# Optimization experiments

Measured on AMD Instinct MI355X. Metric: run time of the kernel, lower is better.

Reference implementation:

```python
import jax, jax.numpy as jnp
import numpy as np
from jax import lax

DN = ('NCHW', 'OIHW', 'NCHW')
BN_EPS = 1e-5


def _conv(x, w, pad):
    # pad: list of (lo, hi) for H, W
    return lax.conv_general_dilated(x, w, (1, 1), pad, dimension_numbers=DN)


def _grid_sample_bilinear(img, grid):
    """F.grid_sample(img, grid, align_corners=True, padding_mode='zeros').
    img: [N,C,H,W], grid: [N,Ho,Wo,2] with (x,y) in [-1,1]."""
    N, C, H, W = img.shape
    gx, gy = grid[..., 0], grid[..., 1]
    # align_corners=True mapping to pixel coords
    ix = (gx + 1.0) * 0.5 * (W - 1)
    iy = (gy + 1.0) * 0.5 * (H - 1)
    x0 = jnp.floor(ix)
    y0 = jnp.floor(iy)
    x1 = x0 + 1.0
    y1 = y0 + 1.0
    # bilinear weights
    wa = (x1 - ix) * (y1 - iy)  # top-left (x0,y0)
    wb = (ix - x0) * (y1 - iy)  # top-right (x1,y0)
    wc = (x1 - ix) * (iy - y0)  # bottom-left (x0,y1)
    wd = (ix - x0) * (iy - y0)  # bottom-right (x1,y1)

    imgc = jnp.transpose(img, (0, 2, 3, 1))  # [N,H,W,C]
    b = jnp.arange(N)[:, None, None]

    def gather(xi, yi):
        valid = (xi >= 0) & (xi <= W - 1) & (yi >= 0) & (yi <= H - 1)
        xc = jnp.clip(xi, 0, W - 1).astype(jnp.int32)
        yc = jnp.clip(yi, 0, H - 1).astype(jnp.int32)
        v = imgc[b, yc, xc]  # [N,Ho,Wo,C]
        return v * valid[..., None].astype(img.dtype)

    out = (gather(x0, y0) * wa[..., None] + gather(x1, y0) * wb[..., None]
           + gather(x0, y1) * wc[..., None] + gather(x1, y1) * wd[..., None])
    return jnp.transpose(out, (0, 3, 1, 2))  # [N,C,Ho,Wo]


def setup_inputs() -> dict:
    key = jax.random.key(0)
    ks = jax.random.split(key, 12)
    N, C1, C2 = 8, 512, 256
    H, W = 64, 64
    x1 = jax.random.normal(ks[0], (N, C1, 2 * H, 2 * W), dtype=jnp.float32)
    x2 = jax.random.normal(ks[1], (N, C2, H, W), dtype=jnp.float32)
    w_change = jax.random.normal(ks[2], (C2, C1, 1, 1), dtype=jnp.float32) * 0.02
    b_change = jax.random.normal(ks[3], (C2,), dtype=jnp.float32) * 0.02
    w_cc1 = jax.random.normal(ks[4], (C2, 2 * C2, 1, 1), dtype=jnp.float32) * 0.02
    bn_gamma = 1.0 + 0.1 * jax.random.normal(ks[5], (C2,), dtype=jnp.float32)
    bn_beta = 0.1 * jax.random.normal(ks[6], (C2,), dtype=jnp.float32)
    bn_mean = 0.1 * jax.random.normal(ks[7], (C2,), dtype=jnp.float32)
    bn_var = jax.random.uniform(ks[8], (C2,), dtype=jnp.float32, minval=0.5, maxval=1.5)
    w_cc2 = jax.random.normal(ks[9], (4, C2, 3, 3), dtype=jnp.float32) * 0.02
    return {"x1": x1, "x2": x2, "w_change": w_change, "b_change": b_change,
            "w_cc1": w_cc1, "bn_gamma": bn_gamma, "bn_beta": bn_beta,
            "bn_mean": bn_mean, "bn_var": bn_var, "w_cc2": w_cc2}


def reference(x1, x2, w_change, b_change, w_cc1, bn_gamma, bn_beta, bn_mean, bn_var, w_cc2):
    # MaxPool2d(2,2)
    x1p = lax.reduce_window(x1, -jnp.inf, lax.max, (1, 1, 2, 2), (1, 1, 2, 2), 'VALID')
    # change: 1x1 conv with bias
    x1c = _conv(x1p, w_change, [(0, 0), (0, 0)]) + b_change[None, :, None, None]
    # concat + concat_conv (1x1 conv -> BN(eval) -> ReLU -> 3x3 conv)
    x = jnp.concatenate([x1c, x2], axis=1)
    x = _conv(x, w_cc1, [(0, 0), (0, 0)])
    inv = lax.rsqrt(bn_var + BN_EPS)
    x = (x - bn_mean[None, :, None, None]) * (inv * bn_gamma)[None, :, None, None] + bn_beta[None, :, None, None]
    x = jax.nn.relu(x)
    flow = _conv(x, w_cc2, [(1, 1), (1, 1)])  # [N,4,H,W]
    flow1 = flow[:, :2]
    flow2 = flow[:, 2:]

    N, _, H, W = x1c.shape
    # base grid: [...,0]=x over width, [...,1]=y over height
    xs = jnp.linspace(-1.0, 1.0, W, dtype=x1c.dtype)
    ys = jnp.linspace(-1.0, 1.0, H, dtype=x1c.dtype)
    base = jnp.stack(jnp.meshgrid(xs, ys, indexing='xy'), axis=-1)  # [H,W,2]
    norm = jnp.array([(W - 1) / 2.0, (H - 1) / 2.0], dtype=x1c.dtype)

    grid1 = base[None] + jnp.transpose(flow1, (0, 2, 3, 1)) / norm
    grid2 = base[None] + jnp.transpose(flow2, (0, 2, 3, 1)) / norm

    u1 = _grid_sample_bilinear(x1c, grid1)
    u2 = _grid_sample_bilinear(x2, grid2)
    return u1 + u2
```

## Files before the change

kernel.cpp:

```cpp
#include <hip/hip_runtime.h>
#include <hip/hip_bf16.h>

#define NB 8
#define C1 512
#define C2 256
#define HWSZ 4096
#define BN_EPS 1e-5f
#define P2 264

typedef __hip_bfloat16 bf16;
typedef __hip_bfloat162 bf162;
typedef __attribute__((ext_vector_type(8))) short short8v;
typedef __attribute__((ext_vector_type(4))) float f32x4;

static __device__ inline float b2f(bf16 h) { return __bfloat162float(h); }

static __device__ inline unsigned short f2bf(float f) {
  union { bf16 h; unsigned short u; } c;
  c.h = __float2bfloat16(f);
  return c.u;
}

static __device__ inline uint2 pack4(float a, float b, float c, float d) {
  union { uint2 u; bf162 h[2]; } pk;
  pk.h[0] = __float22bfloat162_rn(make_float2(a, b));
  pk.h[1] = __float22bfloat162_rn(make_float2(c, d));
  return pk.u;
}

__global__ __launch_bounds__(256) void k0_swizzle(
    const float* __restrict__ wch, const float* __restrict__ wcc1,
    unsigned short* __restrict__ wchB, unsigned short* __restrict__ wcc1B) {
  const int t = blockIdx.x * 256 + threadIdx.x;
  const int which = t >> 17;
  const int r = t & 131071;
  const int i = r & 7;
  const int lane = (r >> 3) & 63;
  const int ntile = (r >> 9) & 15;
  const int kstep = r >> 13;
  const int ci = kstep * 32 + (lane >> 4) * 8 + i;
  const int co = ntile * 16 + (lane & 15);
  const float* s = which ? wcc1 : wch;
  unsigned short* d = which ? wcc1B : wchB;
  d[r] = f2bf(s[co * 512 + ci]);
}

__global__ __launch_bounds__(256) void k12_fused(
    const float* __restrict__ x1, const float* __restrict__ x2,
    const unsigned short* __restrict__ wchB, const unsigned short* __restrict__ wcc1B,
    const float* __restrict__ bch,
    const float* __restrict__ gamma, const float* __restrict__ beta,
    const float* __restrict__ mean, const float* __restrict__ var,
    bf16* __restrict__ x1c, bf16* __restrict__ xbn) {
  __shared__ unsigned short As[32 * 40];
  __shared__ unsigned short As2[32 * P2];
  const int tid = threadIdx.x;
  const int lane = tid & 63;
  const int wv = tid >> 6;
  const int lrow = lane & 15;
  const int lgrp = lane >> 4;
  const int sm = tid & 31;
  const int skq = tid >> 5;

  const int m0g = blockIdx.x * 32;
  const int n = m0g >> 12;
  const int hw0 = m0g & 4095;
  const int h = hw0 >> 6;
  const int w0 = hw0 & 63;

  f32x4 acc[2][4];
#pragma unroll
  for (int mt = 0; mt < 2; ++mt)
#pragma unroll
    for (int nt = 0; nt < 4; ++nt) acc[mt][nt] = (f32x4){0.f, 0.f, 0.f, 0.f};

  const size_t x1base = ((size_t)n * C1 * 16384) + (size_t)(2 * h) * 128 + (size_t)(2 * (w0 + sm));

  float av[4];
#pragma unroll
  for (int j = 0; j < 4; ++j) {
    const size_t cioff = (size_t)(skq * 4 + j) * 16384;
    const float2 p0 = *(const float2*)(x1 + x1base + cioff);
    const float2 p1 = *(const float2*)(x1 + x1base + cioff + 128);
    av[j] = fmaxf(fmaxf(p0.x, p0.y), fmaxf(p1.x, p1.y));
  }

  for (int ks = 0; ks < 16; ++ks) {
    __syncthreads();
    *(uint2*)&As[sm * 40 + skq * 4] = pack4(av[0], av[1], av[2], av[3]);
    __syncthreads();

    const short8v a0 = *(const short8v*)&As[lrow * 40 + lgrp * 8];
    const short8v a1 = *(const short8v*)&As[(16 + lrow) * 40 + lgrp * 8];

    if (ks < 15) {
      const int k0 = (ks + 1) * 32;
#pragma unroll
      for (int j = 0; j < 4; ++j) {
        const size_t cioff = (size_t)(k0 + skq * 4 + j) * 16384;
        const float2 p0 = *(const float2*)(x1 + x1base + cioff);
        const float2 p1 = *(const float2*)(x1 + x1base + cioff + 128);
        av[j] = fmaxf(fmaxf(p0.x, p0.y), fmaxf(p1.x, p1.y));
      }
    }

#pragma unroll
    for (int nt = 0; nt < 4; ++nt) {
      const int ntile = wv * 4 + nt;
      const short8v b = *(const short8v*)&wchB[(size_t)((ks * 16 + ntile) * 64 + lane) * 8];
      acc[0][nt] = __builtin_amdgcn_mfma_f32_16x16x32_bf16(a0, b, acc[0][nt], 0, 0, 0);
      acc[1][nt] = __builtin_amdgcn_mfma_f32_16x16x32_bf16(a1, b, acc[1][nt], 0, 0, 0);
    }
  }

#pragma unroll
  for (int nt = 0; nt < 4; ++nt) {
    const int co = wv * 64 + nt * 16 + lrow;
    const float bias = bch[co];
#pragma unroll
    for (int mt = 0; mt < 2; ++mt) {
      const f32x4 v = acc[mt][nt];
      const uint2 pk = pack4(v.x + bias, v.y + bias, v.z + bias, v.w + bias);
      *(uint2*)&x1c[((size_t)(n * C2 + co)) * HWSZ + hw0 + mt * 16 + lgrp * 4] = pk;
      const int mb = mt * 16 + lgrp * 4;
      As2[(mb + 0) * P2 + co] = (unsigned short)(pk.x & 0xffffu);
      As2[(mb + 1) * P2 + co] = (unsigned short)(pk.x >> 16);
      As2[(mb + 2) * P2 + co] = (unsigned short)(pk.y & 0xffffu);
      As2[(mb + 3) * P2 + co] = (unsigned short)(pk.y >> 16);
      acc[mt][nt] = (f32x4){0.f, 0.f, 0.f, 0.f};
    }
  }
  __syncthreads();

  const int ch = tid >> 3;
  const int mq = (tid & 7) * 4;

  float4 cf = *(const float4*)&x2[((size_t)(n * C2 + ch)) * HWSZ + hw0 + mq];

#pragma unroll
  for (int ks = 0; ks < 8; ++ks) {
    const short8v a0 = *(const short8v*)&As2[lrow * P2 + ks * 32 + lgrp * 8];
    const short8v a1 = *(const short8v*)&As2[(16 + lrow) * P2 + ks * 32 + lgrp * 8];
#pragma unroll
    for (int nt = 0; nt < 4; ++nt) {
      const int ntile = wv * 4 + nt;
      const short8v b = *(const short8v*)&wcc1B[(size_t)((ks * 16 + ntile) * 64 + lane) * 8];
      acc[0][nt] = __builtin_amdgcn_mfma_f32_16x16x32_bf16(a0, b, acc[0][nt], 0, 0, 0);
      acc[1][nt] = __builtin_amdgcn_mfma_f32_16x16x32_bf16(a1, b, acc[1][nt], 0, 0, 0);
    }
  }

  for (int ks = 8; ks < 16; ++ks) {
    unsigned short pk[4];
    pk[0] = f2bf(cf.x); pk[1] = f2bf(cf.y); pk[2] = f2bf(cf.z); pk[3] = f2bf(cf.w);
    if (ks < 15) {
      cf = *(const float4*)&x2[((size_t)(n * C2 + (ks - 7) * 32 + ch)) * HWSZ + hw0 + mq];
    }
    __syncthreads();
    As[(mq + 0) * 40 + ch] = pk[0];
    As[(mq + 1) * 40 + ch] = pk[1];
    As[(mq + 2) * 40 + ch] = pk[2];
    As[(mq + 3) * 40 + ch] = pk[3];
    __syncthreads();

    const short8v a0 = *(const short8v*)&As[lrow * 40 + lgrp * 8];
    const short8v a1 = *(const short8v*)&As[(16 + lrow) * 40 + lgrp * 8];
#pragma unroll
    for (int nt = 0; nt < 4; ++nt) {
      const int ntile = wv * 4 + nt;
      const short8v b = *(const short8v*)&wcc1B[(size_t)((ks * 16 + ntile) * 64 + lane) * 8];
      acc[0][nt] = __builtin_amdgcn_mfma_f32_16x16x32_bf16(a0, b, acc[0][nt], 0, 0, 0);
      acc[1][nt] = __builtin_amdgcn_mfma_f32_16x16x32_bf16(a1, b, acc[1][nt], 0, 0, 0);
    }
  }

#pragma unroll
  for (int nt = 0; nt < 4; ++nt) {
    const int co = wv * 64 + nt * 16 + lrow;
    const float sc = gamma[co] * rsqrtf(var[co] + BN_EPS);
    const float sh = beta[co] - mean[co] * sc;
#pragma unroll
    for (int mt = 0; mt < 2; ++mt) {
      const f32x4 vv = acc[mt][nt];
      *(uint2*)&xbn[((size_t)(n * C2 + co)) * HWSZ + hw0 + mt * 16 + lgrp * 4] =
          pack4(fmaxf(vv.x * sc + sh, 0.f), fmaxf(vv.y * sc + sh, 0.f),
                fmaxf(vv.z * sc + sh, 0.f), fmaxf(vv.w * sc + sh, 0.f));
    }
  }
}

__global__ __launch_bounds__(1024) void k34_conv_sample(
    const bf16* __restrict__ xbn, const float* __restrict__ wcc2,
    const bf16* __restrict__ x1c, const float* __restrict__ x2,
    float* __restrict__ out) {
  __shared__ float wsm[9216];
  __shared__ float part[16][4][64];
  __shared__ float flr[4][64];
  const int tid = threadIdx.x;
  const int n = blockIdx.x >> 6;
  const int h = blockIdx.x & 63;
  const int wl = tid & 63;
  const int q = tid >> 6;

  for (int idx = tid; idx < 9216; idx += 1024) {
    const int f = idx / 2304;
    const int r = idx % 2304;
    const int ci = r / 9;
    const int t = r % 9;
    wsm[ci * 36 + (t / 3) * 12 + (t % 3) * 4 + f] = wcc2[idx];
  }
  __syncthreads();

  float acc[4] = {0.f, 0.f, 0.f, 0.f};
  {
    const bf16* base = xbn + ((size_t)(n * C2 + q * 16)) * HWSZ;
    const float* wq = wsm + (q * 16) * 36;
    for (int cc = 0; cc < 16; ++cc) {
      const bf16* src = base + (size_t)cc * HWSZ;
      const float* wc = wq + cc * 36;
#pragma unroll
      for (int dy = 0; dy < 3; ++dy) {
        const int y = h + dy - 1;
        if ((unsigned)y >= 64u) continue;
        const float v = b2f(src[y * 64 + wl]);
        float vm = __shfl_up(v, 1);
        float vp = __shfl_down(v, 1);
        if (wl == 0) vm = 0.f;
        if (wl == 63) vp = 0.f;
        const float4 wa = *(const float4*)&wc[dy * 12 + 0];
        const float4 wb = *(const float4*)&wc[dy * 12 + 4];
        const float4 wd = *(const float4*)&wc[dy * 12 + 8];
        acc[0] = fmaf(vm, wa.x, fmaf(v, wb.x, fmaf(vp, wd.x, acc[0])));
        acc[1] = fmaf(vm, wa.y, fmaf(v, wb.y, fmaf(vp, wd.y, acc[1])));
        acc[2] = fmaf(vm, wa.z, fmaf(v, wb.z, fmaf(vp, wd.z, acc[2])));
        acc[3] = fmaf(vm, wa.w, fmaf(v, wb.w, fmaf(vp, wd.w, acc[3])));
      }
    }
  }
  part[q][0][wl] = acc[0];
  part[q][1][wl] = acc[1];
  part[q][2][wl] = acc[2];
  part[q][3][wl] = acc[3];
  __syncthreads();
  if (tid < 256) {
    const int f = tid >> 6;
    const int ww = tid & 63;
    float s = 0.f;
#pragma unroll
    for (int qq = 0; qq < 16; ++qq) s += part[qq][f][ww];
    flr[f][ww] = s;
  }
  __syncthreads();

  const float fx1 = flr[0][wl];
  const float fy1 = flr[1][wl];
  const float fx2 = flr[2][wl];
  const float fy2 = flr[3][wl];

  int oA1, oB1, oC1, oD1; float wa1, wb1, wc1, wd1;
  {
    const float ix = (float)wl + fx1, iy = (float)h + fy1;
    const float x0f = floorf(ix), y0f = floorf(iy);
    const float fx = ix - x0f, fy = iy - y0f;
    const int x0 = (int)x0f, y0 = (int)y0f, x1i = x0 + 1, y1i = y0 + 1;
    const float vx0 = (x0 >= 0 && x0 < 64) ? 1.f : 0.f;
    const float vx1 = (x1i >= 0 && x1i < 64) ? 1.f : 0.f;
    const float vy0 = (y0 >= 0 && y0 < 64) ? 1.f : 0.f;
    const float vy1 = (y1i >= 0 && y1i < 64) ? 1.f : 0.f;
    const int cx0 = min(max(x0, 0), 63), cx1 = min(max(x1i, 0), 63);
    const int cy0 = min(max(y0, 0), 63), cy1 = min(max(y1i, 0), 63);
    oA1 = cy0 * 64 + cx0; oB1 = cy0 * 64 + cx1;
    oC1 = cy1 * 64 + cx0; oD1 = cy1 * 64 + cx1;
    wa1 = (1.f - fx) * (1.f - fy) * vx0 * vy0;
    wb1 = fx * (1.f - fy) * vx1 * vy0;
    wc1 = (1.f - fx) * fy * vx0 * vy1;
    wd1 = fx * fy * vx1 * vy1;
  }
  int oA2, oB2, oC2, oD2; float wa2, wb2, wc2, wd2;
  {
    const float ix = (float)wl + fx2, iy = (float)h + fy2;
    const float x0f = floorf(ix), y0f = floorf(iy);
    const float fx = ix - x0f, fy = iy - y0f;
    const int x0 = (int)x0f, y0 = (int)y0f, x1i = x0 + 1, y1i = y0 + 1;
    const float vx0 = (x0 >= 0 && x0 < 64) ? 1.f : 0.f;
    const float vx1 = (x1i >= 0 && x1i < 64) ? 1.f : 0.f;
    const float vy0 = (y0 >= 0 && y0 < 64) ? 1.f : 0.f;
    const float vy1 = (y1i >= 0 && y1i < 64) ? 1.f : 0.f;
    const int cx0 = min(max(x0, 0), 63), cx1 = min(max(x1i, 0), 63);
    const int cy0 = min(max(y0, 0), 63), cy1 = min(max(y1i, 0), 63);
    oA2 = cy0 * 64 + cx0; oB2 = cy0 * 64 + cx1;
    oC2 = cy1 * 64 + cx0; oD2 = cy1 * 64 + cx1;
    wa2 = (1.f - fx) * (1.f - fy) * vx0 * vy0;
    wb2 = fx * (1.f - fy) * vx1 * vy0;
    wc2 = (1.f - fx) * fy * vx0 * vy1;
    wd2 = fx * fy * vx1 * vy1;
  }

  const bf16*  p1 = x1c + ((size_t)n * C2) * HWSZ;
  const float* p2 = x2 + ((size_t)n * C2) * HWSZ;
  const size_t obase = ((size_t)n * C2) * HWSZ + h * 64 + wl;
#pragma unroll 4
  for (int i = 0; i < 16; ++i) {
    const int co = q * 16 + i;
    const bf16*  q1 = p1 + (size_t)co * HWSZ;
    const float* q2 = p2 + (size_t)co * HWSZ;
    const float u = b2f(q1[oA1]) * wa1 + b2f(q1[oB1]) * wb1 + b2f(q1[oC1]) * wc1 + b2f(q1[oD1]) * wd1
                  + q2[oA2] * wa2 + q2[oB2] * wb2 + q2[oC2] * wc2 + q2[oD2] * wd2;
    out[obase + (size_t)co * HWSZ] = u;
  }
}

extern "C" void kernel_launch(void* const* d_in, const int* in_sizes, int n_in,
                              void* d_out, int out_size, void* d_ws, size_t ws_size,
                              hipStream_t stream) {
  const float* x1      = (const float*)d_in[0];
  const float* x2      = (const float*)d_in[1];
  const float* w_change= (const float*)d_in[2];
  const float* b_change= (const float*)d_in[3];
  const float* w_cc1   = (const float*)d_in[4];
  const float* bn_gamma= (const float*)d_in[5];
  const float* bn_beta = (const float*)d_in[6];
  const float* bn_mean = (const float*)d_in[7];
  const float* bn_var  = (const float*)d_in[8];
  const float* w_cc2   = (const float*)d_in[9];
  float* out = (float*)d_out;

  bf16*           x1c   = (bf16*)d_ws;
  bf16*           xbn   = (bf16*)((char*)d_ws + (16u << 20));
  unsigned short* wchB  = (unsigned short*)((char*)d_ws + (32u << 20));
  unsigned short* wcc1B = (unsigned short*)((char*)d_ws + (32u << 20) + (256u << 10));

  k0_swizzle<<<1024, 256, 0, stream>>>(w_change, w_cc1, wchB, wcc1B);
  k12_fused<<<1024, 256, 0, stream>>>(x1, x2, wchB, wcc1B, b_change,
                                      bn_gamma, bn_beta, bn_mean, bn_var,
                                      x1c, xbn);
  k34_conv_sample<<<512, 1024, 0, stream>>>(xbn, w_cc2, x1c, x2, out);
}
```

Measured before the change: 150.4 us.

## Deepen x1/x2 prefetch to two stages and use raw LDS barriers in fused GEMM

```diff
diff --git a/kernel.cpp b/kernel.cpp
--- a/kernel.cpp
+++ b/kernel.cpp
@@ -21,12 +21,22 @@
   return c.u;
 }
 
+static __device__ inline unsigned pack2(float a, float b) {
+  union { unsigned u; bf162 h; } pk;
+  pk.h = __float22bfloat162_rn(make_float2(a, b));
+  return pk.u;
+}
+
 static __device__ inline uint2 pack4(float a, float b, float c, float d) {
   union { uint2 u; bf162 h[2]; } pk;
   pk.h[0] = __float22bfloat162_rn(make_float2(a, b));
   pk.h[1] = __float22bfloat162_rn(make_float2(c, d));
   return pk.u;
 }
+
+#define SBARQ() asm volatile("s_waitcnt lgkmcnt(0)\n\ts_barrier" ::: "memory")
+#define SBAR()  asm volatile("s_barrier" ::: "memory")
+#define LGKM0() asm volatile("s_waitcnt lgkmcnt(0)" ::: "memory")
 
 __global__ __launch_bounds__(256) void k0_swizzle(
     const float* __restrict__ wch, const float* __restrict__ wcc1,
@@ -59,8 +69,6 @@
   const int wv = tid >> 6;
   const int lrow = lane & 15;
   const int lgrp = lane >> 4;
-  const int sm = tid & 31;
-  const int skq = tid >> 5;
 
   const int m0g = blockIdx.x * 32;
   const int n = m0g >> 12;
@@ -74,36 +82,45 @@
 #pragma unroll
     for (int nt = 0; nt < 4; ++nt) acc[mt][nt] = (f32x4){0.f, 0.f, 0.f, 0.f};
 
-  const size_t x1base = ((size_t)n * C1 * 16384) + (size_t)(2 * h) * 128 + (size_t)(2 * (w0 + sm));
-
-  float av[4];
-#pragma unroll
-  for (int j = 0; j < 4; ++j) {
-    const size_t cioff = (size_t)(skq * 4 + j) * 16384;
-    const float2 p0 = *(const float2*)(x1 + x1base + cioff);
-    const float2 p1 = *(const float2*)(x1 + x1base + cioff + 128);
-    av[j] = fmaxf(fmaxf(p0.x, p0.y), fmaxf(p1.x, p1.y));
-  }
+  const int pmi = tid & 15;
+  const int ms = pmi * 2;
+  const int ch0 = (tid >> 4) * 2;
+
+  const float* x1p = x1 + (size_t)n * C1 * 16384 + (size_t)(2 * h) * 128 + 2 * (w0 + ms);
+
+  float4 t0, b0, t1, b1;
+#define LOADA(K0_) do { \
+    const float* p_ = x1p + (size_t)((K0_) + ch0) * 16384; \
+    t0 = *(const float4*)p_;            b0 = *(const float4*)(p_ + 128); \
+    t1 = *(const float4*)(p_ + 16384);  b1 = *(const float4*)(p_ + 16384 + 128); \
+  } while (0)
+#define POOLA(U0_, U1_) do { \
+    U0_ = pack2(fmaxf(fmaxf(t0.x, t0.y), fmaxf(b0.x, b0.y)), \
+                fmaxf(fmaxf(t1.x, t1.y), fmaxf(b1.x, b1.y))); \
+    U1_ = pack2(fmaxf(fmaxf(t0.z, t0.w), fmaxf(b0.z, b0.w)), \
+                fmaxf(fmaxf(t1.z, t1.w), fmaxf(b1.z, b1.w))); \
+  } while (0)
+
+  unsigned uA0, uA1;
+  LOADA(0);
+  POOLA(uA0, uA1);
+  LOADA(32);
 
   for (int ks = 0; ks < 16; ++ks) {
-    __syncthreads();
-    *(uint2*)&As[sm * 40 + skq * 4] = pack4(av[0], av[1], av[2], av[3]);
-    __syncthreads();
+    SBARQ();
+    *(unsigned*)&As[ms * 40 + ch0] = uA0;
+    *(unsigned*)&As[(ms + 1) * 40 + ch0] = uA1;
+    LGKM0();
+    SBAR();
+
+    unsigned uN0, uN1;
+    if (ks < 15) {
+      POOLA(uN0, uN1);
+      if (ks < 14) LOADA((ks + 2) * 32);
+    }
 
     const short8v a0 = *(const short8v*)&As[lrow * 40 + lgrp * 8];
     const short8v a1 = *(const short8v*)&As[(16 + lrow) * 40 + lgrp * 8];
-
-    if (ks < 15) {
-      const int k0 = (ks + 1) * 32;
-#pragma unroll
-      for (int j = 0; j < 4; ++j) {
-        const size_t cioff = (size_t)(k0 + skq * 4 + j) * 16384;
-        const float2 p0 = *(const float2*)(x1 + x1base + cioff);
-        const float2 p1 = *(const float2*)(x1 + x1base + cioff + 128);
-        av[j] = fmaxf(fmaxf(p0.x, p0.y), fmaxf(p1.x, p1.y));
-      }
-    }
-
 #pragma unroll
     for (int nt = 0; nt < 4; ++nt) {
       const int ntile = wv * 4 + nt;
@@ -111,7 +128,13 @@
       acc[0][nt] = __builtin_amdgcn_mfma_f32_16x16x32_bf16(a0, b, acc[0][nt], 0, 0, 0);
       acc[1][nt] = __builtin_amdgcn_mfma_f32_16x16x32_bf16(a1, b, acc[1][nt], 0, 0, 0);
     }
-  }
+    if (ks < 15) { uA0 = uN0; uA1 = uN1; }
+  }
+
+  const int chB = tid >> 3;
+  const int mqB = (tid & 7) * 4;
+  float4 cf0 = *(const float4*)&x2[((size_t)(n * C2 + chB)) * HWSZ + hw0 + mqB];
+  float4 cf1 = *(const float4*)&x2[((size_t)(n * C2 + 32 + chB)) * HWSZ + hw0 + mqB];
 
 #pragma unroll
   for (int nt = 0; nt < 4; ++nt) {
@@ -130,12 +153,8 @@
       acc[mt][nt] = (f32x4){0.f, 0.f, 0.f, 0.f};
     }
   }
-  __syncthreads();
-
-  const int ch = tid >> 3;
-  const int mq = (tid & 7) * 4;
-
-  float4 cf = *(const float4*)&x2[((size_t)(n * C2 + ch)) * HWSZ + hw0 + mq];
+  LGKM0();
+  SBAR();
 
 #pragma unroll
   for (int ks = 0; ks < 8; ++ks) {
@@ -151,17 +170,19 @@
   }
 
   for (int ks = 8; ks < 16; ++ks) {
-    unsigned short pk[4];
-    pk[0] = f2bf(cf.x); pk[1] = f2bf(cf.y); pk[2] = f2bf(cf.z); pk[3] = f2bf(cf.w);
-    if (ks < 15) {
-      cf = *(const float4*)&x2[((size_t)(n * C2 + (ks - 7) * 32 + ch)) * HWSZ + hw0 + mq];
-    }
-    __syncthreads();
-    As[(mq + 0) * 40 + ch] = pk[0];
-    As[(mq + 1) * 40 + ch] = pk[1];
-    As[(mq + 2) * 40 + ch] = pk[2];
-    As[(mq + 3) * 40 + ch] = pk[3];
-    __syncthreads();
+    const unsigned p0 = pack2(cf0.x, cf0.y);
+    const unsigned p1 = pack2(cf0.z, cf0.w);
+    cf0 = cf1;
+    if (ks < 14) {
+      cf1 = *(const float4*)&x2[((size_t)(n * C2 + (ks - 6) * 32 + chB)) * HWSZ + hw0 + mqB];
+    }
+    SBARQ();
+    As[(mqB + 0) * 40 + chB] = (unsigned short)(p0 & 0xffffu);
+    As[(mqB + 1) * 40 + chB] = (unsigned short)(p0 >> 16);
+    As[(mqB + 2) * 40 + chB] = (unsigned short)(p1 & 0xffffu);
+    As[(mqB + 3) * 40 + chB] = (unsigned short)(p1 >> 16);
+    LGKM0();
+    SBAR();
 
     const short8v a0 = *(const short8v*)&As[lrow * 40 + lgrp * 8];
     const short8v a1 = *(const short8v*)&As[(16 + lrow) * 40 + lgrp * 8];
@@ -187,6 +208,8 @@
                 fmaxf(vv.z * sc + sh, 0.f), fmaxf(vv.w * sc + sh, 0.f));
     }
   }
+#undef LOADA
+#undef POOLA
 }
 
 __global__ __launch_bounds__(1024) void k34_conv_sample(
```

Result: faster. 146.2 us (-2.8%).
